# Performance work log

Hardware: AMD Instinct MI355X
Metric: run time of the kernel (lower is better)

## Reference

```python
import jax, jax.numpy as jnp
import numpy as np

B, T, C = 2, 2048, 1024
NH = 16
HD = C // NH  # 64
FF = 4 * C
EPS = 1e-5


def layer_norm(x, w, b):
    mu = jnp.mean(x, axis=-1, keepdims=True)
    var = jnp.mean(jnp.square(x - mu), axis=-1, keepdims=True)
    return (x - mu) * jax.lax.rsqrt(var + EPS) * w + b


def setup_inputs() -> dict:
    key = jax.random.key(0)
    ks = jax.random.split(key, 12)
    s_in = 1.0 / np.sqrt(C)
    s_ff = 1.0 / np.sqrt(FF)
    return {
        "x": jax.random.normal(ks[0], (B, T, C), jnp.float32),
        "ln1_w": jnp.ones((C,), jnp.float32),
        "ln1_b": jnp.zeros((C,), jnp.float32),
        "Wq": jax.random.normal(ks[1], (C, C), jnp.float32) * s_in,
        "Wk": jax.random.normal(ks[2], (C, C), jnp.float32) * s_in,
        "Wv": jax.random.normal(ks[3], (C, C), jnp.float32) * s_in,
        "Wp": jax.random.normal(ks[4], (C, C), jnp.float32) * s_in,
        "bp": jnp.zeros((C,), jnp.float32),
        "ln2_w": jnp.ones((C,), jnp.float32),
        "ln2_b": jnp.zeros((C,), jnp.float32),
        "W1": jax.random.normal(ks[5], (C, FF), jnp.float32) * s_in,
        "b1": jnp.zeros((FF,), jnp.float32),
        "W2": jax.random.normal(ks[6], (FF, C), jnp.float32) * s_ff,
        "b2": jnp.zeros((C,), jnp.float32),
    }


def reference(x, ln1_w, ln1_b, Wq, Wk, Wv, Wp, bp, ln2_w, ln2_b, W1, b1, W2, b2):
    scale = HD ** (-0.5)
    h = layer_norm(x, ln1_w, ln1_b)  # [B,T,C]
    # project and split heads: [B,T,NH,HD] -> [B,NH,T,HD]
    q = (h @ Wq).reshape(B, T, NH, HD).transpose(0, 2, 1, 3)
    k = (h @ Wk).reshape(B, T, NH, HD).transpose(0, 2, 1, 3)
    v = (h @ Wv).reshape(B, T, NH, HD).transpose(0, 2, 1, 3)
    scores = jnp.einsum("bhqd,bhkd->bhqk", q, k) * scale  # [B,NH,T,T]
    causal = jnp.tril(jnp.ones((T, T), jnp.bool_))
    scores = jnp.where(causal, scores, -jnp.inf)
    attn = jax.nn.softmax(scores, axis=-1)
    o = jnp.einsum("bhqk,bhkd->bhqd", attn, v)  # [B,NH,T,HD]
    o = o.transpose(0, 2, 1, 3).reshape(B, T, C)
    x = x + o @ Wp + bp
    h2 = layer_norm(x, ln2_w, ln2_b)
    x = x + jax.nn.relu(h2 @ W1 + b1) @ W2 + b2
    return x
```

## Files before the change

### kernel.cpp

```cpp
#include <hip/hip_runtime.h>
#include <hip/hip_bf16.h>

using u16 = unsigned short;
typedef short v8s __attribute__((ext_vector_type(8)));
typedef float v4f __attribute__((ext_vector_type(4)));

#define B_ 2
#define T_ 2048
#define C_ 1024
#define NH_ 16
#define HD_ 64
#define FF_ 4096
#define NT (B_*T_)
#define QKVC 3072

__device__ __forceinline__ u16 f2b(float f) {
  union { float f; unsigned int i; } v; v.f = f;
  unsigned int r = (v.i + 0x7FFFu + ((v.i >> 16) & 1u)) >> 16;
  return (u16)r;
}
__device__ __forceinline__ float b2f(u16 u) {
  union { unsigned int i; float f; } v; v.i = ((unsigned int)u) << 16; return v.f;
}
__device__ __forceinline__ v4f mfma16(v8s a, v8s b, v4f c) {
  return __builtin_amdgcn_mfma_f32_16x16x32_bf16(a, b, c, 0, 0, 0);
}
__device__ __forceinline__ void glds16(const u16* g, u16* l) {
  __builtin_amdgcn_global_load_lds(
      (const __attribute__((address_space(1))) unsigned int*)g,
      (__attribute__((address_space(3))) unsigned int*)l, 16, 0, 0);
}

__global__ __launch_bounds__(256) void wcvt_kernel(const float* __restrict__ W,
    u16* __restrict__ Wt, int K, int N) {
  __shared__ float t[32][33];
  int tx = threadIdx.x & 31, ty = threadIdx.x >> 5;
  int n0 = blockIdx.x * 32, k0 = blockIdx.y * 32;
#pragma unroll
  for (int j = 0; j < 4; ++j)
    t[ty + j * 8][tx] = W[(size_t)(k0 + ty + j * 8) * N + n0 + tx];
  __syncthreads();
#pragma unroll
  for (int j = 0; j < 4; ++j)
    Wt[(size_t)(n0 + ty + j * 8) * K + k0 + tx] = f2b(t[tx][ty + j * 8]);
}

__global__ __launch_bounds__(256) void ln_kernel(const float* __restrict__ x,
    const float* __restrict__ w, const float* __restrict__ b, u16* __restrict__ y) {
  int row = blockIdx.x;
  int tid = threadIdx.x;
  const float* xr = x + (size_t)row * C_;
  float4 f4 = *(const float4*)&xr[tid * 4];
  float f[4] = {f4.x, f4.y, f4.z, f4.w};
  float s1 = 0.f, s2 = 0.f;
#pragma unroll
  for (int i = 0; i < 4; ++i) { s1 += f[i]; s2 += f[i] * f[i]; }
#pragma unroll
  for (int off = 32; off > 0; off >>= 1) {
    s1 += __shfl_down(s1, off);
    s2 += __shfl_down(s2, off);
  }
  __shared__ float red[10];
  int lane = tid & 63, wid = tid >> 6;
  if (lane == 0) { red[wid] = s1; red[4 + wid] = s2; }
  __syncthreads();
  if (tid == 0) {
    float a = red[0] + red[1] + red[2] + red[3];
    float q = red[4] + red[5] + red[6] + red[7];
    float mu = a * (1.f / C_);
    float var = q * (1.f / C_) - mu * mu;
    red[8] = mu; red[9] = rsqrtf(var + 1e-5f);
  }
  __syncthreads();
  float mu = red[8], rs = red[9];
  union { uint2 v; u16 s[4]; } st;
#pragma unroll
  for (int i = 0; i < 4; ++i) {
    int c = tid * 4 + i;
    st.s[i] = f2b((f[i] - mu) * rs * w[c] + b[c]);
  }
  *(uint2*)&y[(size_t)row * C_ + tid * 4] = st.v;
}

__global__ __launch_bounds__(256) void gemm_bt(const u16* __restrict__ X,
    const u16* __restrict__ Wt, const float* __restrict__ bias,
    const float* __restrict__ resf, u16* __restrict__ Yb, float* __restrict__ Yf,
    float* __restrict__ Yfz1, int M, int N, int lda, int ldb, int kspl, int relu) {
  __shared__ __align__(16) u16 As[2][128 * 32];
  __shared__ __align__(16) u16 Bs[2][128 * 32];
  int tid = threadIdx.x, lane = tid & 63, w = tid >> 6;
  int wm = w >> 1, wn = w & 1, quad = lane >> 4, lcol = lane & 15;
  int m0 = blockIdx.y * 128, n0 = blockIdx.x * 128;
  int koff = blockIdx.z * kspl;
  v4f acc[4][4] = {};
  int sr = lane >> 2, sc = lane & 3;
  const u16* gA = X  + (size_t)(m0 + w * 32 + sr) * lda + koff + sc * 8;
  const u16* gB = Wt + (size_t)(n0 + w * 32 + sr) * ldb + koff + sc * 8;
  u16* lA0 = As[0] + (w * 32) * 32;
  u16* lA1 = As[1] + (w * 32) * 32;
  u16* lB0 = Bs[0] + (w * 32) * 32;
  u16* lB1 = Bs[1] + (w * 32) * 32;
  for (int k0 = 0; k0 < kspl; k0 += 64) {
    __syncthreads();
    glds16(gA + k0,                        lA0);
    glds16(gA + k0 + (size_t)16 * lda,     lA0 + 16 * 32);
    glds16(gA + k0 + 32,                   lA1);
    glds16(gA + k0 + 32 + (size_t)16 * lda, lA1 + 16 * 32);
    glds16(gB + k0,                        lB0);
    glds16(gB + k0 + (size_t)16 * ldb,     lB0 + 16 * 32);
    glds16(gB + k0 + 32,                   lB1);
    glds16(gB + k0 + 32 + (size_t)16 * ldb, lB1 + 16 * 32);
    __syncthreads();
#pragma unroll
    for (int kh = 0; kh < 2; ++kh) {
      v8s a[4], b[4];
#pragma unroll
      for (int i = 0; i < 4; ++i) {
        a[i] = *(v8s*)&As[kh][(wm * 64 + i * 16 + lcol) * 32 + quad * 8];
        b[i] = *(v8s*)&Bs[kh][(wn * 64 + i * 16 + lcol) * 32 + quad * 8];
      }
#pragma unroll
      for (int i = 0; i < 4; ++i)
#pragma unroll
        for (int j = 0; j < 4; ++j)
          acc[i][j] = mfma16(a[i], b[j], acc[i][j]);
    }
  }
  float* yf = blockIdx.z ? Yfz1 : Yf;
#pragma unroll
  for (int i = 0; i < 4; ++i) {
    int mb = m0 + wm * 64 + i * 16 + quad * 4;
#pragma unroll
    for (int j = 0; j < 4; ++j) {
      int n = n0 + wn * 64 + j * 16 + lcol;
#pragma unroll
      for (int r = 0; r < 4; ++r) {
        float v = acc[i][j][r];
        if (bias) v += bias[n];
        if (resf) v += resf[(size_t)(mb + r) * N + n];
        if (relu) v = fmaxf(v, 0.f);
        if (Yb) Yb[(size_t)(mb + r) * N + n] = f2b(v);
        else    yf[(size_t)(mb + r) * N + n] = v;
      }
    }
  }
}

__global__ __launch_bounds__(256) void gemm_bt_n64(const u16* __restrict__ X,
    const u16* __restrict__ Wt, const float* __restrict__ bias,
    const float* __restrict__ resf, u16* __restrict__ Yb, float* __restrict__ Yf,
    int M, int N, int K, int relu) {
  __shared__ __align__(16) u16 As[2][128 * 32];
  __shared__ __align__(16) u16 Bs[2][64 * 32];
  int tid = threadIdx.x, lane = tid & 63, w = tid >> 6;
  int wm = w >> 1, wn = w & 1, quad = lane >> 4, lcol = lane & 15;
  int m0 = blockIdx.y * 128, n0 = blockIdx.x * 64;
  v4f acc[4][2] = {};
  int sr = lane >> 2, sc = lane & 3;
  const u16* gA = X  + (size_t)(m0 + w * 32 + sr) * K + sc * 8;
  const u16* gB = Wt + (size_t)(n0 + w * 16 + sr) * K + sc * 8;
  u16* lA0 = As[0] + (w * 32) * 32;
  u16* lA1 = As[1] + (w * 32) * 32;
  u16* lB0 = Bs[0] + (w * 16) * 32;
  u16* lB1 = Bs[1] + (w * 16) * 32;
  for (int k0 = 0; k0 < K; k0 += 64) {
    __syncthreads();
    glds16(gA + k0,                       lA0);
    glds16(gA + k0 + (size_t)16 * K,      lA0 + 16 * 32);
    glds16(gA + k0 + 32,                  lA1);
    glds16(gA + k0 + 32 + (size_t)16 * K, lA1 + 16 * 32);
    glds16(gB + k0,                       lB0);
    glds16(gB + k0 + 32,                  lB1);
    __syncthreads();
#pragma unroll
    for (int kh = 0; kh < 2; ++kh) {
      v8s a[4], b[2];
#pragma unroll
      for (int i = 0; i < 4; ++i)
        a[i] = *(v8s*)&As[kh][(wm * 64 + i * 16 + lcol) * 32 + quad * 8];
#pragma unroll
      for (int j = 0; j < 2; ++j)
        b[j] = *(v8s*)&Bs[kh][(wn * 32 + j * 16 + lcol) * 32 + quad * 8];
#pragma unroll
      for (int i = 0; i < 4; ++i)
#pragma unroll
        for (int j = 0; j < 2; ++j)
          acc[i][j] = mfma16(a[i], b[j], acc[i][j]);
    }
  }
#pragma unroll
  for (int i = 0; i < 4; ++i) {
    int mb = m0 + wm * 64 + i * 16 + quad * 4;
#pragma unroll
    for (int j = 0; j < 2; ++j) {
      int n = n0 + wn * 32 + j * 16 + lcol;
#pragma unroll
      for (int r = 0; r < 4; ++r) {
        float v = acc[i][j][r];
        if (bias) v += bias[n];
        if (resf) v += resf[(size_t)(mb + r) * N + n];
        if (relu) v = fmaxf(v, 0.f);
        if (Yb) Yb[(size_t)(mb + r) * N + n] = f2b(v);
        else    Yf[(size_t)(mb + r) * N + n] = v;
      }
    }
  }
}

__global__ __launch_bounds__(256) void add4_kernel(float* __restrict__ out,
    const float* __restrict__ p0, const float* __restrict__ bias,
    const float* __restrict__ res) {
  size_t e0 = ((size_t)blockIdx.x * 256 + threadIdx.x) * 4;
  int col = (int)(e0 & (C_ - 1));
  float4 o = *(float4*)&out[e0];
  float4 p = *(const float4*)&p0[e0];
  float4 r = *(const float4*)&res[e0];
  float4 bb = *(const float4*)&bias[col];
  o.x += p.x + r.x + bb.x;
  o.y += p.y + r.y + bb.y;
  o.z += p.z + r.z + bb.z;
  o.w += p.w + r.w + bb.w;
  *(float4*)&out[e0] = o;
}

__global__ __launch_bounds__(256) void vt_kernel(const u16* __restrict__ QKV,
    u16* __restrict__ VT) {
  int bh = blockIdx.x, tt = blockIdx.y;
  int b = bh >> 4, h = bh & 15;
  int tid = threadIdx.x;
  __shared__ u16 L[64 * 72];
  int r = tid >> 2, g = tid & 3;
  size_t row = ((size_t)(b * T_ + tt * 64 + r)) * QKVC + 2 * C_ + h * HD_;
  union { uint4 v; u16 s[8]; } a0, a1;
  a0.v = *(const uint4*)&QKV[row + g * 8];
  a1.v = *(const uint4*)&QKV[row + 32 + g * 8];
#pragma unroll
  for (int e = 0; e < 8; ++e) L[(g * 8 + e) * 72 + r] = a0.s[e];
#pragma unroll
  for (int e = 0; e < 8; ++e) L[(32 + g * 8 + e) * 72 + r] = a1.s[e];
  __syncthreads();
  size_t orow = ((size_t)(bh * 64 + r)) * T_ + tt * 64;
  *(uint4*)&VT[orow + g * 8]      = *(uint4*)&L[r * 72 + g * 8];
  *(uint4*)&VT[orow + 32 + g * 8] = *(uint4*)&L[r * 72 + 32 + g * 8];
}

__global__ __launch_bounds__(256) void attn_kernel(const u16* __restrict__ QKV,
    const u16* __restrict__ VT, u16* __restrict__ Opart, float* __restrict__ lpart) {
  int bh = blockIdx.x, y = blockIdx.y, z = blockIdx.z;
  int b = bh >> 4, h = bh & 15;
  int tid = threadIdx.x, lane = tid & 63, wid = tid >> 6;
  int quad = lane >> 4, lcol = lane & 15;
  __shared__ __align__(16) u16 Ps[4][32 * 72];
  const float SC = 0.125f * 1.44269504f;
  const float EB = 8.0f * 1.44269504f;
  const u16* kbase = QKV + (size_t)b * T_ * QKVC + C_ + h * HD_;
  const u16* vbase = VT + (size_t)(bh * 64) * T_;
  u16* psw = Ps[wid];
  u16* Os = Opart + (size_t)z * NT * C_;
  float* ls = lpart + (size_t)z * 32 * T_;

  auto ldk = [&](v8s (&ak)[4][2], int kb) {
#pragma unroll
    for (int cg = 0; cg < 4; ++cg)
#pragma unroll
      for (int kh = 0; kh < 2; ++kh)
        ak[cg][kh] = *(const v8s*)&kbase[(size_t)(kb * 64 + cg * 16 + lcol) * QKVC + kh * 32 + quad * 8];
  };

#pragma unroll
  for (int pi = 0; pi < 2; ++pi) {
    int qt = pi ? (15 - y) : y;
    int qg[2];
    v8s bq[2][2];
#pragma unroll
    for (int j = 0; j < 2; ++j) {
      qg[j] = qt * 128 + wid * 32 + j * 16 + lcol;
#pragma unroll
      for (int kh = 0; kh < 2; ++kh)
        bq[j][kh] = *(const v8s*)&QKV[(size_t)(b * T_ + qg[j]) * QKVC + h * HD_ + kh * 32 + quad * 8];
    }
    float l_i[2] = {0.f, 0.f};
    v4f accO[4][2] = {};
    int kbmax = 2 * qt + (wid >> 1);
    int mid = (kbmax + 2) >> 1;
    int lo = z ? mid : 0;
    int hi = z ? kbmax : (mid - 1);

    auto ctile = [&](v8s (&ak)[4][2], int kb, bool diag) {
      v8s av[4][2];
#pragma unroll
      for (int df = 0; df < 4; ++df)
#pragma unroll
        for (int kh = 0; kh < 2; ++kh)
          av[df][kh] = *(const v8s*)&vbase[(size_t)(df * 16 + lcol) * T_ + kb * 64 + kh * 32 + quad * 8];
#pragma unroll
      for (int j = 0; j < 2; ++j) {
        v4f s[4];
#pragma unroll
        for (int cg = 0; cg < 4; ++cg) {
          v4f acc = {};
          acc = mfma16(ak[cg][1], bq[j][1], acc);
          s[cg] = mfma16(ak[cg][0], bq[j][0], acc);
        }
        float ps = 0.f;
#pragma unroll
        for (int cg = 0; cg < 4; ++cg) {
          union { u16 s4[4]; unsigned long long ll; } pk;
#pragma unroll
          for (int rg = 0; rg < 4; ++rg) {
            float pv = exp2f(s[cg][rg] * SC - EB);
            if (diag) {
              int kt = kb * 64 + cg * 16 + quad * 4 + rg;
              pv = (kt <= qg[j]) ? pv : 0.f;
            }
            ps += pv;
            pk.s4[rg] = f2b(pv);
          }
          *(unsigned long long*)&psw[(j * 16 + lcol) * 72 + cg * 16 + quad * 4] = pk.ll;
        }
        ps += __shfl_xor(ps, 16);
        ps += __shfl_xor(ps, 32);
        l_i[j] += ps;
        v8s bp0 = *(v8s*)&psw[(j * 16 + lcol) * 72 + quad * 8];
        v8s bp1 = *(v8s*)&psw[(j * 16 + lcol) * 72 + 32 + quad * 8];
#pragma unroll
        for (int df = 0; df < 4; ++df) {
          v4f t = mfma16(av[df][1], bp1, accO[df][j]);
          accO[df][j] = mfma16(av[df][0], bp0, t);
        }
      }
    };

    if (lo <= hi) {
      v8s a0k[4][2], a1k[4][2];
      ldk(a0k, lo);
      for (int kb = lo; kb <= hi; kb += 2) {
        if (kb + 1 <= hi) ldk(a1k, kb + 1);
        ctile(a0k, kb, kb == kbmax);
        if (kb + 1 <= hi) {
          if (kb + 2 <= hi) ldk(a0k, kb + 2);
          ctile(a1k, kb + 1, (kb + 1) == kbmax);
        }
      }
    }
#pragma unroll
    for (int j = 0; j < 2; ++j) {
      float inv = (l_i[j] > 0.f) ? (1.f / l_i[j]) : 0.f;
      size_t orow = ((size_t)(b * T_ + qg[j])) * C_ + h * HD_;
      if (quad == 0) ls[bh * T_ + qg[j]] = l_i[j];
#pragma unroll
      for (int df = 0; df < 4; ++df) {
        union { u16 s4[4]; unsigned long long ll; } ok;
#pragma unroll
        for (int rg = 0; rg < 4; ++rg) ok.s4[rg] = f2b(accO[df][j][rg] * inv);
        *(unsigned long long*)&Os[orow + df * 16 + quad * 4] = ok.ll;
      }
    }
  }
}

__global__ __launch_bounds__(256) void ared_kernel(const u16* __restrict__ Opart,
    const float* __restrict__ lpart, u16* __restrict__ Ob) {
  size_t e0 = ((size_t)blockIdx.x * 256 + threadIdx.x) * 4;
  int tb = (int)(e0 >> 10);
  int col = (int)(e0 & (C_ - 1));
  int bq = tb >> 11, t = tb & (T_ - 1);
  int h = col >> 6;
  int lidx = (bq * 16 + h) * T_ + t;
  float l0 = lpart[lidx], l1 = lpart[32 * T_ + lidx];
  float inv = 1.f / (l0 + l1);
  float w0 = l0 * inv, w1 = l1 * inv;
  union { uint2 v; u16 s[4]; } a, b, o;
  a.v = *(const uint2*)&Opart[e0];
  b.v = *(const uint2*)&Opart[(size_t)NT * C_ + e0];
#pragma unroll
  for (int i = 0; i < 4; ++i)
    o.s[i] = f2b(b2f(a.s[i]) * w0 + b2f(b.s[i]) * w1);
  *(uint2*)&Ob[e0] = o.v;
}

extern "C" void kernel_launch(void* const* d_in, const int* in_sizes, int n_in,
                              void* d_out, int out_size, void* d_ws, size_t ws_size,
                              hipStream_t stream) {
  (void)in_sizes; (void)n_in; (void)out_size; (void)ws_size;
  const float* x    = (const float*)d_in[0];
  const float* ln1w = (const float*)d_in[1];
  const float* ln1b = (const float*)d_in[2];
  const float* Wq   = (const float*)d_in[3];
  const float* Wk   = (const float*)d_in[4];
  const float* Wv   = (const float*)d_in[5];
  const float* Wp   = (const float*)d_in[6];
  const float* bp   = (const float*)d_in[7];
  const float* ln2w = (const float*)d_in[8];
  const float* ln2b = (const float*)d_in[9];
  const float* W1   = (const float*)d_in[10];
  const float* b1   = (const float*)d_in[11];
  const float* W2   = (const float*)d_in[12];
  const float* b2   = (const float*)d_in[13];
  float* out = (float*)d_out;
  char* ws = (char*)d_ws;
  const size_t MB = 1024 * 1024;
  u16*   h1    = (u16*)(ws);
  u16*   VT    = (u16*)(ws);
  u16*   QKVb  = (u16*)(ws + 8  * MB);
  u16*   Ob    = (u16*)(ws + 32 * MB);
  float* xa    = (float*)(ws + 40 * MB);
  u16*   Opart = (u16*)(ws + 40 * MB);
  u16*   h2    = (u16*)(ws);
  u16*   f1    = (u16*)(ws + 8 * MB);
  u16*   Wqkvt = (u16*)(ws + 56 * MB);
  float* lpart = (float*)(ws + 56 * MB);
  u16*   Wpt   = (u16*)(ws + 62 * MB);
  u16*   W1t   = (u16*)(ws + 64 * MB);
  u16*   W2t   = (u16*)(ws + 72 * MB);
  float* p0    = (float*)(ws + 56 * MB);

  wcvt_kernel<<<dim3(32, 32),  256, 0, stream>>>(Wq, Wqkvt,                1024, 1024);
  wcvt_kernel<<<dim3(32, 32),  256, 0, stream>>>(Wk, Wqkvt + 1024 * 1024,  1024, 1024);
  wcvt_kernel<<<dim3(32, 32),  256, 0, stream>>>(Wv, Wqkvt + 2048 * 1024,  1024, 1024);
  wcvt_kernel<<<dim3(32, 32),  256, 0, stream>>>(Wp, Wpt,                  1024, 1024);
  wcvt_kernel<<<dim3(128, 32), 256, 0, stream>>>(W1, W1t,                  1024, 4096);
  wcvt_kernel<<<dim3(32, 128), 256, 0, stream>>>(W2, W2t,                  4096, 1024);

  ln_kernel<<<NT, 256, 0, stream>>>(x, ln1w, ln1b, h1);
  gemm_bt<<<dim3(QKVC / 128, NT / 128, 1), 256, 0, stream>>>(
      h1, Wqkvt, nullptr, nullptr, QKVb, nullptr, nullptr, NT, QKVC, C_, C_, C_, 0);
  vt_kernel<<<dim3(B_ * NH_, T_ / 64), 256, 0, stream>>>(QKVb, VT);
  attn_kernel<<<dim3(B_ * NH_, T_ / 256, 2), 256, 0, stream>>>(QKVb, VT, Opart, lpart);
  ared_kernel<<<(NT * C_) / (256 * 4), 256, 0, stream>>>(Opart, lpart, Ob);
  gemm_bt_n64<<<dim3(C_ / 64, NT / 128), 256, 0, stream>>>(
      Ob, Wpt, bp, x, nullptr, xa, NT, C_, C_, 0);
  ln_kernel<<<NT, 256, 0, stream>>>(xa, ln2w, ln2b, h2);
  gemm_bt<<<dim3(FF_ / 128, NT / 128, 1), 256, 0, stream>>>(
      h2, W1t, b1, nullptr, f1, nullptr, nullptr, NT, FF_, C_, C_, C_, 1);
  gemm_bt<<<dim3(C_ / 128, NT / 128, 2), 256, 0, stream>>>(
      f1, W2t, nullptr, nullptr, nullptr, p0, out, NT, C_, FF_, FF_, FF_ / 2, 0);
  add4_kernel<<<(NT * C_) / (256 * 4), 256, 0, stream>>>(out, p0, b2, xa);
}
```

Baseline: 448.0 us.

## Restructure attention into per-wave 64-row query tiles with three-way strided KV split

The attention kernel now gives each wave its own 64-row query tile (qt = wid*8 + blockIdx.y) and splits the key blocks three ways with a stride-3 loop over blockIdx.z, instead of pairing query tiles per block and splitting KV into halves. The reduction kernel merges three partial outputs, and the partial buffer moves to 32MB so all three fit in the workspace. P values are converted to bf16 by truncation rather than rounding, and launch bounds request 3 blocks per CU. The aim is more parallelism and higher occupancy. The cost is that the K register double-buffering is dropped, and waves in a block now have very unequal causal work, so each block waits on its longest wave.

```diff
diff --git a/kernel.cpp b/kernel.cpp
--- a/kernel.cpp
+++ b/kernel.cpp
@@ -18,6 +18,10 @@
   union { float f; unsigned int i; } v; v.f = f;
   unsigned int r = (v.i + 0x7FFFu + ((v.i >> 16) & 1u)) >> 16;
   return (u16)r;
+}
+__device__ __forceinline__ u16 f2bt(float f) {
+  union { float f; unsigned int i; } v; v.f = f;
+  return (u16)(v.i >> 16);
 }
 __device__ __forceinline__ float b2f(u16 u) {
   union { unsigned int i; float f; } v; v.i = ((unsigned int)u) << 16; return v.f;
@@ -244,57 +248,45 @@
   *(uint4*)&VT[orow + 32 + g * 8] = *(uint4*)&L[r * 72 + 32 + g * 8];
 }
 
-__global__ __launch_bounds__(256) void attn_kernel(const u16* __restrict__ QKV,
+__global__ __launch_bounds__(256, 3) void attn_kernel(const u16* __restrict__ QKV,
     const u16* __restrict__ VT, u16* __restrict__ Opart, float* __restrict__ lpart) {
-  int bh = blockIdx.x, y = blockIdx.y, z = blockIdx.z;
+  int bh = blockIdx.x, g = blockIdx.y, z = blockIdx.z;
   int b = bh >> 4, h = bh & 15;
   int tid = threadIdx.x, lane = tid & 63, wid = tid >> 6;
   int quad = lane >> 4, lcol = lane & 15;
-  __shared__ __align__(16) u16 Ps[4][32 * 72];
+  __shared__ __align__(16) u16 Ps[4][4 * 16 * 72];
   const float SC = 0.125f * 1.44269504f;
   const float EB = 8.0f * 1.44269504f;
+  int qt = wid * 8 + g;
   const u16* kbase = QKV + (size_t)b * T_ * QKVC + C_ + h * HD_;
   const u16* vbase = VT + (size_t)(bh * 64) * T_;
   u16* psw = Ps[wid];
   u16* Os = Opart + (size_t)z * NT * C_;
   float* ls = lpart + (size_t)z * 32 * T_;
 
-  auto ldk = [&](v8s (&ak)[4][2], int kb) {
-#pragma unroll
-    for (int cg = 0; cg < 4; ++cg)
-#pragma unroll
-      for (int kh = 0; kh < 2; ++kh)
-        ak[cg][kh] = *(const v8s*)&kbase[(size_t)(kb * 64 + cg * 16 + lcol) * QKVC + kh * 32 + quad * 8];
-  };
-
-#pragma unroll
-  for (int pi = 0; pi < 2; ++pi) {
-    int qt = pi ? (15 - y) : y;
-    int qg[2];
-    v8s bq[2][2];
-#pragma unroll
-    for (int j = 0; j < 2; ++j) {
-      qg[j] = qt * 128 + wid * 32 + j * 16 + lcol;
-#pragma unroll
-      for (int kh = 0; kh < 2; ++kh)
-        bq[j][kh] = *(const v8s*)&QKV[(size_t)(b * T_ + qg[j]) * QKVC + h * HD_ + kh * 32 + quad * 8];
-    }
-    float l_i[2] = {0.f, 0.f};
-    v4f accO[4][2] = {};
-    int kbmax = 2 * qt + (wid >> 1);
-    int mid = (kbmax + 2) >> 1;
-    int lo = z ? mid : 0;
-    int hi = z ? kbmax : (mid - 1);
-
-    auto ctile = [&](v8s (&ak)[4][2], int kb, bool diag) {
-      v8s av[4][2];
-#pragma unroll
-      for (int df = 0; df < 4; ++df)
+  int qg[4];
+  v8s bq[4][2];
+#pragma unroll
+  for (int j = 0; j < 4; ++j) {
+    qg[j] = qt * 64 + j * 16 + lcol;
+#pragma unroll
+    for (int kh = 0; kh < 2; ++kh)
+      bq[j][kh] = *(const v8s*)&QKV[(size_t)(b * T_ + qg[j]) * QKVC + h * HD_ + kh * 32 + quad * 8];
+  }
+  float l_i[4] = {0.f, 0.f, 0.f, 0.f};
+  v4f accO[4][4] = {};
+
+  for (int kb = z; kb <= qt; kb += 3) {
+    bool diag = (kb == qt);
+    {
+      v8s ak[4][2];
+#pragma unroll
+      for (int cg = 0; cg < 4; ++cg)
 #pragma unroll
         for (int kh = 0; kh < 2; ++kh)
-          av[df][kh] = *(const v8s*)&vbase[(size_t)(df * 16 + lcol) * T_ + kb * 64 + kh * 32 + quad * 8];
-#pragma unroll
-      for (int j = 0; j < 2; ++j) {
+          ak[cg][kh] = *(const v8s*)&kbase[(size_t)(kb * 64 + cg * 16 + lcol) * QKVC + kh * 32 + quad * 8];
+#pragma unroll
+      for (int j = 0; j < 4; ++j) {
         v4f s[4];
 #pragma unroll
         for (int cg = 0; cg < 4; ++cg) {
@@ -314,47 +306,43 @@
               pv = (kt <= qg[j]) ? pv : 0.f;
             }
             ps += pv;
-            pk.s4[rg] = f2b(pv);
+            pk.s4[rg] = f2bt(pv);
           }
-          *(unsigned long long*)&psw[(j * 16 + lcol) * 72 + cg * 16 + quad * 4] = pk.ll;
+          *(unsigned long long*)&psw[j * 1152 + lcol * 72 + cg * 16 + quad * 4] = pk.ll;
         }
         ps += __shfl_xor(ps, 16);
         ps += __shfl_xor(ps, 32);
         l_i[j] += ps;
-        v8s bp0 = *(v8s*)&psw[(j * 16 + lcol) * 72 + quad * 8];
-        v8s bp1 = *(v8s*)&psw[(j * 16 + lcol) * 72 + 32 + quad * 8];
-#pragma unroll
-        for (int df = 0; df < 4; ++df) {
-          v4f t = mfma16(av[df][1], bp1, accO[df][j]);
-          accO[df][j] = mfma16(av[df][0], bp0, t);
-        }
       }
-    };
-
-    if (lo <= hi) {
-      v8s a0k[4][2], a1k[4][2];
-      ldk(a0k, lo);
-      for (int kb = lo; kb <= hi; kb += 2) {
-        if (kb + 1 <= hi) ldk(a1k, kb + 1);
-        ctile(a0k, kb, kb == kbmax);
-        if (kb + 1 <= hi) {
-          if (kb + 2 <= hi) ldk(a0k, kb + 2);
-          ctile(a1k, kb + 1, (kb + 1) == kbmax);
-        }
+    }
+    v8s av[4][2];
+#pragma unroll
+    for (int df = 0; df < 4; ++df)
+#pragma unroll
+      for (int kh = 0; kh < 2; ++kh)
+        av[df][kh] = *(const v8s*)&vbase[(size_t)(df * 16 + lcol) * T_ + kb * 64 + kh * 32 + quad * 8];
+#pragma unroll
+    for (int j = 0; j < 4; ++j) {
+      v8s bp0 = *(v8s*)&psw[j * 1152 + lcol * 72 + quad * 8];
+      v8s bp1 = *(v8s*)&psw[j * 1152 + lcol * 72 + 32 + quad * 8];
+#pragma unroll
+      for (int df = 0; df < 4; ++df) {
+        v4f t = mfma16(av[df][1], bp1, accO[df][j]);
+        accO[df][j] = mfma16(av[df][0], bp0, t);
       }
     }
-#pragma unroll
-    for (int j = 0; j < 2; ++j) {
-      float inv = (l_i[j] > 0.f) ? (1.f / l_i[j]) : 0.f;
-      size_t orow = ((size_t)(b * T_ + qg[j])) * C_ + h * HD_;
-      if (quad == 0) ls[bh * T_ + qg[j]] = l_i[j];
-#pragma unroll
-      for (int df = 0; df < 4; ++df) {
-        union { u16 s4[4]; unsigned long long ll; } ok;
-#pragma unroll
-        for (int rg = 0; rg < 4; ++rg) ok.s4[rg] = f2b(accO[df][j][rg] * inv);
-        *(unsigned long long*)&Os[orow + df * 16 + quad * 4] = ok.ll;
-      }
+  }
+#pragma unroll
+  for (int j = 0; j < 4; ++j) {
+    float inv = (l_i[j] > 0.f) ? (1.f / l_i[j]) : 0.f;
+    size_t orow = ((size_t)(b * T_ + qg[j])) * C_ + h * HD_;
+    if (quad == 0) ls[bh * T_ + qg[j]] = l_i[j];
+#pragma unroll
+    for (int df = 0; df < 4; ++df) {
+      union { u16 s4[4]; unsigned long long ll; } ok;
+#pragma unroll
+      for (int rg = 0; rg < 4; ++rg) ok.s4[rg] = f2b(accO[df][j][rg] * inv);
+      *(unsigned long long*)&Os[orow + df * 16 + quad * 4] = ok.ll;
     }
   }
 }
@@ -367,15 +355,18 @@
   int bq = tb >> 11, t = tb & (T_ - 1);
   int h = col >> 6;
   int lidx = (bq * 16 + h) * T_ + t;
-  float l0 = lpart[lidx], l1 = lpart[32 * T_ + lidx];
-  float inv = 1.f / (l0 + l1);
-  float w0 = l0 * inv, w1 = l1 * inv;
-  union { uint2 v; u16 s[4]; } a, b, o;
+  float l0 = lpart[lidx];
+  float l1 = lpart[32 * T_ + lidx];
+  float l2 = lpart[64 * T_ + lidx];
+  float inv = 1.f / (l0 + l1 + l2);
+  float w0 = l0 * inv, w1 = l1 * inv, w2 = l2 * inv;
+  union { uint2 v; u16 s[4]; } a, b, c, o;
   a.v = *(const uint2*)&Opart[e0];
   b.v = *(const uint2*)&Opart[(size_t)NT * C_ + e0];
+  c.v = *(const uint2*)&Opart[(size_t)2 * NT * C_ + e0];
 #pragma unroll
   for (int i = 0; i < 4; ++i)
-    o.s[i] = f2b(b2f(a.s[i]) * w0 + b2f(b.s[i]) * w1);
+    o.s[i] = f2b(b2f(a.s[i]) * w0 + b2f(b.s[i]) * w1 + b2f(c.s[i]) * w2);
   *(uint2*)&Ob[e0] = o.v;
 }
 
@@ -404,8 +395,8 @@
   u16*   VT    = (u16*)(ws);
   u16*   QKVb  = (u16*)(ws + 8  * MB);
   u16*   Ob    = (u16*)(ws + 32 * MB);
+  u16*   Opart = (u16*)(ws + 32 * MB);
   float* xa    = (float*)(ws + 40 * MB);
-  u16*   Opart = (u16*)(ws + 40 * MB);
   u16*   h2    = (u16*)(ws);
   u16*   f1    = (u16*)(ws + 8 * MB);
   u16*   Wqkvt = (u16*)(ws + 56 * MB);
@@ -426,7 +417,7 @@
   gemm_bt<<<dim3(QKVC / 128, NT / 128, 1), 256, 0, stream>>>(
       h1, Wqkvt, nullptr, nullptr, QKVb, nullptr, nullptr, NT, QKVC, C_, C_, C_, 0);
   vt_kernel<<<dim3(B_ * NH_, T_ / 64), 256, 0, stream>>>(QKVb, VT);
-  attn_kernel<<<dim3(B_ * NH_, T_ / 256, 2), 256, 0, stream>>>(QKVb, VT, Opart, lpart);
+  attn_kernel<<<dim3(B_ * NH_, 8, 3), 256, 0, stream>>>(QKVb, VT, Opart, lpart);
   ared_kernel<<<(NT * C_) / (256 * 4), 256, 0, stream>>>(Opart, lpart, Ob);
   gemm_bt_n64<<<dim3(C_ / 64, NT / 128), 256, 0, stream>>>(
       Ob, Wpt, bp, x, nullptr, xa, NT, C_, C_, 0);
```

Measured after the change: 430.2 us. -4.0%, faster.
